# Optimization experiments

Hardware: AMD Instinct MI355X
Metric: run time of the kernel (lower is better)

The kernel has to match this reference:

```python
import jax, jax.numpy as jnp
import numpy as np

BN_EPS = 1e-5
K_NEIGHBOR = 30
NUM_GRAPH = 4


def _bn_lrelu(x, g, b, axes):
    # BatchNorm in training mode (batch stats, biased var) + LeakyReLU(0.2).
    mean = jnp.mean(x, axes, keepdims=True)
    var = jnp.var(x, axes, keepdims=True)
    y = (x - mean) * jax.lax.rsqrt(var + BN_EPS) * g + b
    return jnp.where(y > 0, y, 0.2 * y)


def _pairwise_distance(pc):
    # pc: (B, N, C) -> (B, N, N) squared euclidean distances
    inner = -2.0 * jnp.einsum('bnc,bmc->bnm', pc, pc)
    sq = jnp.sum(pc * pc, axis=-1, keepdims=True)
    return sq + inner + jnp.swapaxes(sq, 1, 2)


def _knn(adj, k):
    return jax.lax.top_k(-adj, k)[1]  # (B, N, k)


def _edge_feature(pc, idx):
    # pc: (B, N, C), idx: (B, N, k) -> (B, N, k, 2C)
    B = pc.shape[0]
    nbrs = pc[jnp.arange(B)[:, None, None], idx]          # (B, N, k, C)
    central = jnp.broadcast_to(pc[:, :, None, :], nbrs.shape)
    return jnp.concatenate([central, nbrs - central], axis=-1)


def _forward(input_image, w64, g64, b64, w128, g128, b128, w1024, g1024, b1024,
             fc1_w, fc1_b, fc2_w, fc2_b, tw, tb,
             wo1, go1, bo1, wo2, go2, bo2, wo3, go3, bo3,
             w1, g1, b1, w2, g2, b2, w3, g3, b3):
    pc = jnp.transpose(input_image, (0, 2, 1))            # (B, N, 3)
    k = K_NEIGHBOR

    # ---- input transform net ----
    idx = _knn(_pairwise_distance(pc), k)
    ef = _edge_feature(pc, idx)                           # (B, N, k, 6)
    net = _bn_lrelu(ef @ w64.T, g64, b64, (0, 1, 2))      # (B, N, k, 64)
    net = _bn_lrelu(net @ w128.T, g128, b128, (0, 1, 2))  # (B, N, k, 128)
    net = jnp.max(net, axis=2)                            # (B, N, 128)
    net = _bn_lrelu(net @ w1024.T, g1024, b1024, (0, 1))  # (B, N, 1024)
    net = jnp.max(net, axis=1)                            # (B, 1024)
    net = net @ fc1_w.T + fc1_b
    net = net @ fc2_w.T + fc2_b                           # (B, 256)
    transform = net @ tw + (jnp.eye(3, dtype=jnp.float32).reshape(-1) + tb)
    transform = transform.reshape(-1, 3, 3)               # (B, 3, 3)

    pct = pc @ transform                                  # (B, N, 3)

    # ---- feature extraction on transformed cloud ----
    idx = _knn(_pairwise_distance(pct), k)
    ef = _edge_feature(pct, idx)                          # (B, N, k, 6)
    out1 = _bn_lrelu(ef @ wo1.T, go1, bo1, (0, 1, 2))     # (B, N, k, 64)
    out2 = _bn_lrelu(out1 @ wo2.T, go2, bo2, (0, 1, 2))   # (B, N, k, 64)
    nmax = jnp.max(out2, axis=2)
    nmean = jnp.mean(out2, axis=2)
    cat1 = jnp.concatenate([nmax, nmean], axis=-1)        # (B, N, 128)
    out3 = _bn_lrelu(cat1 @ wo3.T, go3, bo3, (0, 1))      # (B, N, 64)

    # ---- num_graph dynamic-graph blocks ----
    out5s, maxs, means = [], [], []
    for _ in range(NUM_GRAPH):
        IF = jnp.concatenate([pct, out3], axis=-1)        # (B, N, 67)
        trans1 = _bn_lrelu(IF @ w1.T, g1, b1, (0, 1))     # (B, N, 3)
        idx = _knn(_pairwise_distance(trans1), k)
        ef = _edge_feature(IF, idx)                       # (B, N, k, 134)
        out4 = _bn_lrelu(ef @ w2.T, g2, b2, (0, 1, 2))    # (B, N, k, 16)
        nm2 = jnp.max(out4, axis=2)                       # (B, N, 16)
        ne2 = jnp.mean(out4, axis=2)
        o5 = jnp.concatenate([nm2, ne2], axis=-1)         # (B, N, 32)
        out5 = _bn_lrelu(o5 @ w3.T, g3, b3, (0, 1))       # (B, N, 16)
        out5s.append(out5); maxs.append(nm2); means.append(ne2)

    def _pack(xs):
        x = jnp.concatenate(xs, axis=-1)                  # (B, N, 64)
        return jnp.transpose(x, (0, 2, 1))[..., None]     # (B, 64, N, 1)

    return (_pack(out5s), _pack(maxs), _pack(means))


def setup_inputs() -> dict:
    key = jax.random.key(0)
    ks = iter(jax.random.split(key, 64))
    def w(shape, s=0.05):
        return jax.random.normal(next(ks), shape, jnp.float32) * s
    B, N = 4, 2048
    inp = {'input_image': jax.random.normal(next(ks), (B, 3, N), jnp.float32)}
    for name, shp in [('w64', (64, 6)), ('w128', (128, 64)), ('w1024', (1024, 128)),
                      ('wo1', (64, 6)), ('wo2', (64, 64)), ('wo3', (64, 128)),
                      ('w1', (3, 67)), ('w2', (16, 134)), ('w3', (16, 32))]:
        inp[name] = w(shp)
        c = shp[0]
        inp['g' + name[1:]] = jnp.ones((c,), jnp.float32)
        inp['b' + name[1:]] = jnp.zeros((c,), jnp.float32)
    inp['fc1_w'] = w((512, 1024)); inp['fc1_b'] = jnp.zeros((512,), jnp.float32)
    inp['fc2_w'] = w((256, 512)); inp['fc2_b'] = jnp.zeros((256,), jnp.float32)
    inp['tw'] = w((256, 9)); inp['tb'] = w((9,))
    return inp


def reference(input_image, w64, g64, b64, w128, g128, b128, w1024, g1024, b1024,
              fc1_w, fc1_b, fc2_w, fc2_b, tw, tb,
              wo1, go1, bo1, wo2, go2, bo2, wo3, go3, bo3,
              w1, g1, b1, w2, g2, b2, w3, g3, b3):
    return _forward(input_image, w64, g64, b64, w128, g128, b128, w1024, g1024, b1024,
                    fc1_w, fc1_b, fc2_w, fc2_b, tw, tb,
                    wo1, go1, bo1, wo2, go2, bo2, wo3, go3, bo3,
                    w1, g1, b1, w2, g2, b2, w3, g3, b3)
```

## Files before the change

### kernel.cpp

```cpp
#include <hip/hip_runtime.h>


#define DEV __device__ __forceinline__
DEV float lrelu(float y) { return y > 0.f ? y : 0.2f * y; }
DEV unsigned fmap(float x) {
  unsigned u = __float_as_uint(x);
  return (u & 0x80000000u) ? ~u : (u | 0x80000000u);
}
DEV float funmap(unsigned m) {
  unsigned u = (m & 0x80000000u) ? (m & 0x7FFFFFFFu) : ~m;
  return __uint_as_float(u);
}

__global__ void zero_kernel(float* p, int n) {
  int id = blockIdx.x * 256 + threadIdx.x;
  if (id < n) p[id] = 0.f;
}

__global__ void iminit_kernel(unsigned* maxm, unsigned* minm) {
  int id = blockIdx.x * 256 + threadIdx.x;
  if (id < 4096) { maxm[id] = 0u; minm[id] = 0xFFFFFFFFu; }
}

__global__ void pc_kernel(const float* __restrict__ in, float* __restrict__ pc) {
  int id = blockIdx.x * 256 + threadIdx.x;
  if (id >= 4 * 3 * 2048) return;
  int n = id & 2047;
  int c = (id >> 11) % 3;
  int b = id / (3 * 2048);
  pc[((b << 11) + n) * 3 + c] = in[id];
}

__global__ __launch_bounds__(256) void knn_kernel(const float* __restrict__ pts, int* __restrict__ idx_out) {
  int tid = threadIdx.x;
  int w = tid >> 6, lane = tid & 63;
  int bn = (blockIdx.x << 2) + w;
  int b = bn >> 11;
  const float* base = pts + (b << 11) * 3;
  double qx = pts[bn * 3 + 0], qy = pts[bn * 3 + 1], qz = pts[bn * 3 + 2];
  double sqn = qx * qx + qy * qy + qz * qz;
  double d[32];
  double cmin = 1e300; int cpos = 0x7fffffff;
#pragma unroll
  for (int i = 0; i < 32; ++i) {
    int m = lane + (i << 6);
    double px = base[m * 3 + 0], py = base[m * 3 + 1], pz = base[m * 3 + 2];
    double v = sqn - 2.0 * (qx * px + qy * py + qz * pz) + (px * px + py * py + pz * pz);
    d[i] = v;
    if (v < cmin) { cmin = v; cpos = m; }
  }
  unsigned rmask = 0u;
  int* out = idx_out + bn * 30;
  for (int it = 0; it < 30; ++it) {
    double gv = cmin; int gp = cpos;
#pragma unroll
    for (int off = 1; off < 64; off <<= 1) {
      double ov = __shfl_xor(gv, off, 64);
      int op = __shfl_xor(gp, off, 64);
      if (ov < gv || (ov == gv && op < gp)) { gv = ov; gp = op; }
    }
    if (lane == 0) out[it] = gp;
    if (lane == (gp & 63)) {
      rmask |= 1u << (gp >> 6);
      cmin = 1e300; cpos = 0x7fffffff;
#pragma unroll
      for (int i = 0; i < 32; ++i) {
        double v = ((rmask >> i) & 1u) ? 1e300 : d[i];
        if (v < cmin) { cmin = v; cpos = lane + (i << 6); }
      }
    }
  }
}

__global__ __launch_bounds__(256) void mom6_kernel(const float* __restrict__ pts, const int* __restrict__ idx,
                                                   double* __restrict__ acc) {
  __shared__ double sred[4][27];
  int tid = threadIdx.x;
  int lane = tid & 63, w = tid >> 6;
  double m[27];
#pragma unroll
  for (int i = 0; i < 27; ++i) m[i] = 0.0;
  int stride = gridDim.x << 8;
  for (int e = (blockIdx.x << 8) + tid; e < 245760; e += stride) {
    int bn = e / 30; int b = bn >> 11;
    int nb = idx[e];
    const float* cen = pts + bn * 3;
    const float* nbp = pts + ((b << 11) + nb) * 3;
    float f[6];
    f[0] = cen[0]; f[1] = cen[1]; f[2] = cen[2];
    f[3] = nbp[0] - f[0]; f[4] = nbp[1] - f[1]; f[5] = nbp[2] - f[2];
    int t = 6;
#pragma unroll
    for (int i = 0; i < 6; ++i) {
      m[i] += f[i];
#pragma unroll
      for (int j = i; j < 6; ++j) m[t++] += (double)f[i] * f[j];
    }
  }
#pragma unroll
  for (int i = 0; i < 27; ++i) {
    double v = m[i];
    v += __shfl_xor(v, 1, 64); v += __shfl_xor(v, 2, 64); v += __shfl_xor(v, 4, 64);
    v += __shfl_xor(v, 8, 64); v += __shfl_xor(v, 16, 64); v += __shfl_xor(v, 32, 64);
    m[i] = v;
  }
  if (lane == 0) {
#pragma unroll
    for (int i = 0; i < 27; ++i) sred[w][i] = m[i];
  }
  __syncthreads();
  if (tid < 27) atomicAdd(&acc[tid], sred[0][tid] + sred[1][tid] + sred[2][tid] + sred[3][tid]);
}

__global__ void finE1_kernel(const double* __restrict__ acc, const float* __restrict__ W,
                             const float* __restrict__ g, const float* __restrict__ bb,
                             float* __restrict__ sc) {
  int c = threadIdx.x;
  if (c >= 64) return;
  double wv[6];
#pragma unroll
  for (int i = 0; i < 6; ++i) wv[i] = W[c * 6 + i];
  double s = 0.0;
#pragma unroll
  for (int i = 0; i < 6; ++i) s += wv[i] * acc[i];
  double q = 0.0; int t = 6;
#pragma unroll
  for (int i = 0; i < 6; ++i)
#pragma unroll
    for (int j = i; j < 6; ++j) {
      double mm = acc[t++];
      q += (i == j) ? wv[i] * wv[i] * mm : 2.0 * wv[i] * wv[j] * mm;
    }
  const double E = 245760.0;
  double mean = s / E;
  double var = q / E - mean * mean;
  if (var < 0) var = 0;
  float sf = g[c] * (float)(1.0 / sqrt(var + 1e-5));
  sc[c] = sf;
  sc[64 + c] = bb[c] - (float)mean * sf;
}

__global__ __launch_bounds__(256) void edgeA_kernel(const float* __restrict__ pts, const int* __restrict__ idx,
                                                    const float* __restrict__ W1, const float* __restrict__ sc1,
                                                    const float* __restrict__ W2,
                                                    float* __restrict__ mxout, float* __restrict__ mnout,
                                                    double* __restrict__ acc) {
  __shared__ double sred[4][64][4];
  int tid = threadIdx.x;
  int lane = tid & 63;
  int wv = tid >> 6;
  int k = lane & 31;
  int bn = (blockIdx.x << 3) + (wv << 1) + (lane >> 5);
  int b = bn >> 11;
  bool valid = k < 30;
  int nb = idx[bn * 30 + (valid ? k : 0)];
  const float* cen = pts + bn * 3;
  const float* nbp = pts + ((b << 11) + nb) * 3;
  float cx = cen[0], cy = cen[1], cz = cen[2];
  float dx = nbp[0] - cx, dy = nbp[1] - cy, dz = nbp[2] - cz;
  float y[64];
#pragma unroll
  for (int j = 0; j < 64; ++j) {
    float x = cx * W1[j * 6 + 0] + cy * W1[j * 6 + 1] + cz * W1[j * 6 + 2]
            + dx * W1[j * 6 + 3] + dy * W1[j * 6 + 4] + dz * W1[j * 6 + 5];
    y[j] = lrelu(fmaf(x, sc1[j], sc1[64 + j]));
  }
  double aS0 = 0.0, aQ0 = 0.0, aS1 = 0.0, aQ1 = 0.0;
  for (int cc = 0; cc < 4; ++cc) {
    float kvx = 0.f, kvn = 0.f;
    for (int q = 0; q < 32; ++q) {
      int c = cc * 32 + q;
      const float* w = W2 + c * 64;
      float a0 = 0.f, a1 = 0.f, a2 = 0.f, a3 = 0.f;
#pragma unroll
      for (int j = 0; j < 64; j += 4) {
        a0 = fmaf(y[j], w[j], a0); a1 = fmaf(y[j + 1], w[j + 1], a1);
        a2 = fmaf(y[j + 2], w[j + 2], a2); a3 = fmaf(y[j + 3], w[j + 3], a3);
      }
      float v = (a0 + a1) + (a2 + a3);
      float vx = valid ? v : -3.4e38f;
      float vn = valid ? v : 3.4e38f;
      float sv = valid ? v : 0.f;
      float sq = valid ? v * v : 0.f;
#pragma unroll
      for (int off = 1; off < 32; off <<= 1) {
        vx = fmaxf(vx, __shfl_xor(vx, off, 64));
        vn = fminf(vn, __shfl_xor(vn, off, 64));
        sv += __shfl_xor(sv, off, 64);
        sq += __shfl_xor(sq, off, 64);
      }
      sv += __shfl_xor(sv, 32, 64);
      sq += __shfl_xor(sq, 32, 64);
      if (k == q) { kvx = vx; kvn = vn; }
      int ol = ((cc & 1) << 5) + q;
      bool own = (lane == ol);
      if (cc < 2) { aS0 += own ? (double)sv : 0.0; aQ0 += own ? (double)sq : 0.0; }
      else        { aS1 += own ? (double)sv : 0.0; aQ1 += own ? (double)sq : 0.0; }
    }
    mxout[bn * 128 + cc * 32 + k] = kvx;
    mnout[bn * 128 + cc * 32 + k] = kvn;
  }
  sred[wv][lane][0] = aS0; sred[wv][lane][1] = aQ0;
  sred[wv][lane][2] = aS1; sred[wv][lane][3] = aQ1;
  __syncthreads();
  int l = tid >> 2, j = tid & 3;
  double t = sred[0][l][j] + sred[1][l][j] + sred[2][l][j] + sred[3][l][j];
  int ch = (j < 2) ? l : 64 + l;
  atomicAdd(&acc[(j & 1) * 128 + ch], t);
}

__global__ void applyA_kernel(const float* __restrict__ mx, const float* __restrict__ mn,
                              const float* __restrict__ sc, float* __restrict__ m128) {
  int id = blockIdx.x * 256 + threadIdx.x;
  if (id >= 8192 * 128) return;
  int c = id & 127;
  float s = sc[c], t = sc[128 + c];
  float sel = (s >= 0.f) ? mx[id] : mn[id];
  m128[id] = lrelu(fmaf(sel, s, t));
}

__global__ __launch_bounds__(256) void statsB_kernel(const float* __restrict__ pts, const int* __restrict__ idx,
                                                     const float* __restrict__ W1, const float* __restrict__ sc1,
                                                     const float* __restrict__ W2, double* __restrict__ acc) {
  __shared__ double sred[4][64][2];
  int tid = threadIdx.x;
  int lane = tid & 63;
  int wv = tid >> 6;
  int k = lane & 31;
  int bn = (blockIdx.x << 3) + (wv << 1) + (lane >> 5);
  int b = bn >> 11;
  bool valid = k < 30;
  int nb = idx[bn * 30 + (valid ? k : 0)];
  const float* cen = pts + bn * 3;
  const float* nbp = pts + ((b << 11) + nb) * 3;
  float cx = cen[0], cy = cen[1], cz = cen[2];
  float dx = nbp[0] - cx, dy = nbp[1] - cy, dz = nbp[2] - cz;
  float y[64];
#pragma unroll
  for (int j = 0; j < 64; ++j) {
    float x = cx * W1[j * 6 + 0] + cy * W1[j * 6 + 1] + cz * W1[j * 6 + 2]
            + dx * W1[j * 6 + 3] + dy * W1[j * 6 + 4] + dz * W1[j * 6 + 5];
    y[j] = lrelu(fmaf(x, sc1[j], sc1[64 + j]));
  }
  double aS = 0.0, aQ = 0.0;
  for (int cc = 0; cc < 2; ++cc) {
    for (int q = 0; q < 32; ++q) {
      int c = cc * 32 + q;
      const float* w = W2 + c * 64;
      float a0 = 0.f, a1 = 0.f, a2 = 0.f, a3 = 0.f;
#pragma unroll
      for (int j = 0; j < 64; j += 4) {
        a0 = fmaf(y[j], w[j], a0); a1 = fmaf(y[j + 1], w[j + 1], a1);
        a2 = fmaf(y[j + 2], w[j + 2], a2); a3 = fmaf(y[j + 3], w[j + 3], a3);
      }
      float v = (a0 + a1) + (a2 + a3);
      float sv = valid ? v : 0.f;
      float sq = valid ? v * v : 0.f;
#pragma unroll
      for (int off = 1; off < 64; off <<= 1) {
        sv += __shfl_xor(sv, off, 64);
        sq += __shfl_xor(sq, off, 64);
      }
      bool own = (lane == c);
      aS += own ? (double)sv : 0.0;
      aQ += own ? (double)sq : 0.0;
    }
  }
  sred[wv][lane][0] = aS; sred[wv][lane][1] = aQ;
  __syncthreads();
  if (tid < 128) {
    int l = tid >> 1, j = tid & 1;
    double t = sred[0][l][j] + sred[1][l][j] + sred[2][l][j] + sred[3][l][j];
    atomicAdd(&acc[j * 64 + l], t);
  }
}

__global__ __launch_bounds__(256) void poolB_kernel(const float* __restrict__ pts, const int* __restrict__ idx,
                                                    const float* __restrict__ W1, const float* __restrict__ sc1,
                                                    const float* __restrict__ W2, const float* __restrict__ sc2,
                                                    float* __restrict__ cat) {
  int tid = threadIdx.x;
  int lane = tid & 63;
  int k = lane & 31;
  int bn = (blockIdx.x << 3) + ((tid >> 6) << 1) + (lane >> 5);
  int b = bn >> 11;
  bool valid = k < 30;
  int nb = idx[bn * 30 + (valid ? k : 0)];
  const float* cen = pts + bn * 3;
  const float* nbp = pts + ((b << 11) + nb) * 3;
  float cx = cen[0], cy = cen[1], cz = cen[2];
  float dx = nbp[0] - cx, dy = nbp[1] - cy, dz = nbp[2] - cz;
  float y[64];
#pragma unroll
  for (int j = 0; j < 64; ++j) {
    float x = cx * W1[j * 6 + 0] + cy * W1[j * 6 + 1] + cz * W1[j * 6 + 2]
            + dx * W1[j * 6 + 3] + dy * W1[j * 6 + 4] + dz * W1[j * 6 + 5];
    y[j] = lrelu(fmaf(x, sc1[j], sc1[64 + j]));
  }
  for (int cc = 0; cc < 2; ++cc) {
    float kvm = 0.f, kvs = 0.f;
    for (int q = 0; q < 32; ++q) {
      int c = cc * 32 + q;
      const float* w = W2 + c * 64;
      float a0 = 0.f, a1 = 0.f, a2 = 0.f, a3 = 0.f;
#pragma unroll
      for (int j = 0; j < 64; j += 4) {
        a0 = fmaf(y[j], w[j], a0); a1 = fmaf(y[j + 1], w[j + 1], a1);
        a2 = fmaf(y[j + 2], w[j + 2], a2); a3 = fmaf(y[j + 3], w[j + 3], a3);
      }
      float v = lrelu(fmaf((a0 + a1) + (a2 + a3), sc2[c], sc2[64 + c]));
      float vm = valid ? v : -3.4e38f;
      float vs = valid ? v : 0.f;
#pragma unroll
      for (int off = 1; off < 32; off <<= 1) {
        vm = fmaxf(vm, __shfl_xor(vm, off, 64));
        vs += __shfl_xor(vs, off, 64);
      }
      if (k == q) { kvm = vm; kvs = vs; }
    }
    cat[bn * 128 + cc * 32 + k] = kvm;
    cat[bn * 128 + 64 + cc * 32 + k] = kvs * (1.f / 30.f);
  }
}

__global__ __launch_bounds__(256) void xo3g_kernel(const float* __restrict__ cat, const float* __restrict__ W3,
                                                   float* __restrict__ xo3T) {
  int tid = threadIdx.x;
  int lane = tid & 63, cw = tid >> 6;
  int bn = (blockIdx.x << 6) + lane;
  const float* cr = cat + bn * 128;
  float a[16];
#pragma unroll
  for (int q = 0; q < 16; ++q) a[q] = 0.f;
  for (int j = 0; j < 128; ++j) {
    float v = cr[j];
#pragma unroll
    for (int q = 0; q < 16; ++q) a[q] += v * W3[(cw * 16 + q) * 128 + j];
  }
#pragma unroll
  for (int q = 0; q < 16; ++q) xo3T[(cw * 16 + q) * 8192 + bn] = a[q];
}

__global__ __launch_bounds__(256) void rstats_kernel(const float* __restrict__ x, int E, int C,
                                                     double* __restrict__ acc) {
  __shared__ double rd[256];
  int c = blockIdx.x, tid = threadIdx.x;
  const float* r = x + (size_t)c * E;
  double ls = 0, lq = 0;
  for (int i = tid; i < E; i += 256) { float v = r[i]; ls += v; lq += (double)v * v; }
  rd[tid] = ls; __syncthreads();
  for (int s = 128; s > 0; s >>= 1) { if (tid < s) rd[tid] += rd[tid + s]; __syncthreads(); }
  if (tid == 0) acc[c] = rd[0];
  __syncthreads();
  rd[tid] = lq; __syncthreads();
  for (int s = 128; s > 0; s >>= 1) { if (tid < s) rd[tid] += rd[tid + s]; __syncthreads(); }
  if (tid == 0) acc[C + c] = rd[0];
}

__global__ __launch_bounds__(256) void cmm1024_kernel(const float* __restrict__ m128, const float* __restrict__ W,
                                                      double* __restrict__ acc, unsigned* __restrict__ maxm,
                                                      unsigned* __restrict__ minm) {
  __shared__ float mt[64 * 132];
  int tid = threadIdx.x;
  int lane = tid & 63;
  int b = blockIdx.x >> 8;
  int cg = (blockIdx.x >> 2) & 63;
  int ns = blockIdx.x & 3;
  int wu = __builtin_amdgcn_readfirstlane(tid >> 6);
  int cbase = cg * 16 + wu * 4;
  const float* wr = W + (size_t)cbase * 128;
  double ls[4] = {0, 0, 0, 0}, lq[4] = {0, 0, 0, 0};
  float mx[4], mn[4];
#pragma unroll
  for (int q = 0; q < 4; ++q) { mx[q] = -3.4e38f; mn[q] = 3.4e38f; }
  for (int ch = 0; ch < 8; ++ch) {
    int n0 = (ns << 9) + (ch << 6);
    __syncthreads();
    for (int i = tid; i < 2048; i += 256) {
      int r = i >> 5, jj = (i & 31) << 2;
      *(float4*)&mt[r * 132 + jj] = *(const float4*)&m128[(size_t)((b << 11) + n0 + r) * 128 + jj];
    }
    __syncthreads();
    float a[4] = {0.f, 0.f, 0.f, 0.f};
    const float* mrow = &mt[lane * 132];
#pragma unroll
    for (int j = 0; j < 128; j += 4) {
      float4 mv = *(const float4*)&mrow[j];
#pragma unroll
      for (int q = 0; q < 4; ++q) {
        const float* wq = wr + q * 128 + j;
        a[q] = fmaf(mv.x, wq[0], a[q]);
        a[q] = fmaf(mv.y, wq[1], a[q]);
        a[q] = fmaf(mv.z, wq[2], a[q]);
        a[q] = fmaf(mv.w, wq[3], a[q]);
      }
    }
#pragma unroll
    for (int q = 0; q < 4; ++q) {
      ls[q] += a[q]; lq[q] += (double)a[q] * a[q];
      mx[q] = fmaxf(mx[q], a[q]); mn[q] = fminf(mn[q], a[q]);
    }
  }
#pragma unroll
  for (int q = 0; q < 4; ++q) {
    double s = ls[q], sq = lq[q];
    float xm = mx[q], xn = mn[q];
    for (int off = 1; off < 64; off <<= 1) {
      s += __shfl_xor(s, off, 64);
      sq += __shfl_xor(sq, off, 64);
      xm = fmaxf(xm, __shfl_xor(xm, off, 64));
      xn = fminf(xn, __shfl_xor(xn, off, 64));
    }
    if (lane == 0) {
      int c = cbase + q;
      atomicAdd(&acc[c], s);
      atomicAdd(&acc[1024 + c], sq);
      atomicMax(&maxm[(b << 10) + c], fmap(xm));
      atomicMin(&minm[(b << 10) + c], fmap(xn));
    }
  }
}

__global__ void fin1024_kernel(const double* __restrict__ acc, const float* __restrict__ g,
                               const float* __restrict__ bb, const unsigned* __restrict__ maxm,
                               const unsigned* __restrict__ minm, float* __restrict__ gmax) {
  int c = blockIdx.x * 256 + threadIdx.x;
  if (c >= 1024) return;
  double mean = acc[c] / 8192.0;
  double var = acc[1024 + c] / 8192.0 - mean * mean;
  if (var < 0) var = 0;
  float s = g[c] * (float)(1.0 / sqrt(var + 1e-5));
  float t = bb[c] - (float)mean * s;
  for (int b = 0; b < 4; ++b) {
    float xm = (s >= 0.f) ? funmap(maxm[(b << 10) + c]) : funmap(minm[(b << 10) + c]);
    gmax[(b << 10) + c] = lrelu(fmaf(xm, s, t));
  }
}

__global__ __launch_bounds__(256) void fc_kernel(const float* __restrict__ gmax,
                                                 const float* __restrict__ fc1w, const float* __restrict__ fc1b,
                                                 const float* __restrict__ fc2w, const float* __restrict__ fc2b,
                                                 const float* __restrict__ tw, const float* __restrict__ tb,
                                                 float* __restrict__ transform) {
  __shared__ float net[1024];
  __shared__ float h1[512];
  __shared__ float h2[256];
  int b = blockIdx.x, tid = threadIdx.x;
  for (int i = tid; i < 1024; i += 256) net[i] = gmax[b * 1024 + i];
  __syncthreads();
  for (int o = tid; o < 512; o += 256) {
    float a = fc1b[o];
    const float* w = fc1w + o * 1024;
    for (int j = 0; j < 1024; ++j) a += net[j] * w[j];
    h1[o] = a;
  }
  __syncthreads();
  {
    int o = tid;
    float a = fc2b[o];
    const float* w = fc2w + o * 512;
    for (int j = 0; j < 512; ++j) a += h1[j] * w[j];
    h2[o] = a;
  }
  __syncthreads();
  if (tid < 9) {
    float a = 0.f;
    for (int i = 0; i < 256; ++i) a += h2[i] * tw[i * 9 + tid];
    float eye = (tid == 0 || tid == 4 || tid == 8) ? 1.f : 0.f;
    transform[b * 9 + tid] = a + eye + tb[tid];
  }
}

__global__ void pct_kernel(const float* __restrict__ pc, const float* __restrict__ T, float* __restrict__ pct) {
  int id = blockIdx.x * 256 + threadIdx.x;
  if (id >= 8192) return;
  int b = id >> 11;
  const float* t = T + b * 9;
  float x = pc[id * 3 + 0], y = pc[id * 3 + 1], z = pc[id * 3 + 2];
  pct[id * 3 + 0] = x * t[0] + y * t[3] + z * t[6];
  pct[id * 3 + 1] = x * t[1] + y * t[4] + z * t[7];
  pct[id * 3 + 2] = x * t[2] + y * t[5] + z * t[8];
}

__global__ __launch_bounds__(256) void dstats_kernel(const float* __restrict__ x, int total, int C,
                                                     double* __restrict__ acc) {
  __shared__ double dred[256];
  int tid = threadIdx.x;
  int c = tid % C;
  double ls = 0, lq = 0;
  int stride = gridDim.x << 8;
  for (int id = (blockIdx.x << 8) + tid; id < total; id += stride) {
    float v = x[id];
    ls += v; lq += (double)v * v;
  }
  dred[tid] = ls; __syncthreads();
  if (tid < C) { double v = 0; for (int i = tid; i < 256; i += C) v += dred[i]; atomicAdd(&acc[c], v); }
  __syncthreads();
  dred[tid] = lq; __syncthreads();
  if (tid < C) { double v = 0; for (int i = tid; i < 256; i += C) v += dred[i]; atomicAdd(&acc[C + c], v); }
}

__global__ __launch_bounds__(256) void stats3_kernel(const float* __restrict__ x, int total, double* __restrict__ acc) {
  __shared__ double dred[256];
  int tid = threadIdx.x;
  double ls[3] = {0, 0, 0}, lq[3] = {0, 0, 0};
  int stride = gridDim.x << 8;
  for (int id = (blockIdx.x << 8) + tid; id < total; id += stride) {
    float v = x[id];
    int c = id % 3;
    ls[c] += v; lq[c] += (double)v * v;
  }
  for (int cc = 0; cc < 3; ++cc) {
    __syncthreads();
    dred[tid] = ls[cc]; __syncthreads();
    for (int s = 128; s > 0; s >>= 1) { if (tid < s) dred[tid] += dred[tid + s]; __syncthreads(); }
    if (tid == 0) atomicAdd(&acc[cc], dred[0]);
    __syncthreads();
    dred[tid] = lq[cc]; __syncthreads();
    for (int s = 128; s > 0; s >>= 1) { if (tid < s) dred[tid] += dred[tid + s]; __syncthreads(); }
    if (tid == 0) atomicAdd(&acc[3 + cc], dred[0]);
  }
}

__global__ void fin_kernel(const double* __restrict__ acc, const float* __restrict__ g, const float* __restrict__ bb,
                           double cnt, int C, float* __restrict__ sc) {
  int c = blockIdx.x * 256 + threadIdx.x;
  if (c >= C) return;
  double mean = acc[c] / cnt;
  double var = acc[C + c] / cnt - mean * mean;
  if (var < 0) var = 0;
  float inv = (float)(1.0 / sqrt(var + 1e-5));
  float s = g[c] * inv;
  sc[c] = s;
  sc[C + c] = bb[c] - (float)mean * s;
}

__global__ void if_kernel(const float* __restrict__ pct, const float* __restrict__ xo3T, const float* __restrict__ sc3,
                          float* __restrict__ IF) {
  int id = blockIdx.x * 256 + threadIdx.x;
  if (id >= 8192 * 67) return;
  int bn = id / 67, j = id % 67;
  float v;
  if (j < 3) v = pct[bn * 3 + j];
  else { int c = j - 3; v = lrelu(fmaf(xo3T[c * 8192 + bn], sc3[c], sc3[64 + c])); }
  IF[id] = v;
}

__global__ void xt1_kernel(const float* __restrict__ IF, const float* __restrict__ W, float* __restrict__ xt1) {
  int id = blockIdx.x * 256 + threadIdx.x;
  if (id >= 8192 * 3) return;
  int bn = id / 3, c = id % 3;
  const float* f = IF + bn * 67;
  const float* w = W + c * 67;
  float a = 0.f;
  for (int j = 0; j < 67; ++j) a += f[j] * w[j];
  xt1[id] = a;
}

__global__ void t1_kernel(const float* __restrict__ xt1, const float* __restrict__ sc, float* __restrict__ trans1) {
  int id = blockIdx.x * 256 + threadIdx.x;
  if (id >= 24576) return;
  int c = id % 3;
  trans1[id] = lrelu(fmaf(xt1[id], sc[c], sc[3 + c]));
}

__global__ __launch_bounds__(256) void x2_kernel(const float* __restrict__ IF, const int* __restrict__ idx,
                                                 const float* __restrict__ W, float* __restrict__ x2,
                                                 double* __restrict__ acc) {
  __shared__ float WT[134 * 16];
  __shared__ double dred[256];
  int tid = threadIdx.x;
  for (int i = tid; i < 134 * 16; i += 256) { int c = i & 15, j = i >> 4; WT[j * 16 + c] = W[c * 134 + j]; }
  __syncthreads();
  int c = tid & 15;
  double ls = 0, lq = 0;
  const int total = 245760 * 16;
  int stride = gridDim.x << 8;
  for (int id = (blockIdx.x << 8) + tid; id < total; id += stride) {
    int p = id >> 4;
    int bn = p / 30; int b = bn >> 11;
    int nb = idx[p];
    const float* cen = IF + (size_t)bn * 67;
    const float* nbp = IF + (size_t)((b << 11) + nb) * 67;
    float a = 0.f;
    for (int j = 0; j < 67; ++j) {
      float cj = cen[j];
      a += cj * WT[j * 16 + c];
      a += (nbp[j] - cj) * WT[(67 + j) * 16 + c];
    }
    x2[id] = a;
    ls += a; lq += (double)a * a;
  }
  dred[tid] = ls; __syncthreads();
  if (tid < 16) { double v = 0; for (int i = tid; i < 256; i += 16) v += dred[i]; atomicAdd(&acc[tid], v); }
  __syncthreads();
  dred[tid] = lq; __syncthreads();
  if (tid < 16) { double v = 0; for (int i = tid; i < 256; i += 16) v += dred[i]; atomicAdd(&acc[16 + tid], v); }
}

__global__ __launch_bounds__(256) void k5_kernel(const float* __restrict__ x2, const float* __restrict__ sc2,
                                                 const float* __restrict__ W3, float* __restrict__ nm2,
                                                 float* __restrict__ ne2, float* __restrict__ x3) {
  __shared__ float W3T[32 * 16];
  __shared__ float o5[4][32];
  int tid = threadIdx.x;
  for (int i = tid; i < 512; i += 256) { int c = i & 15, j = i >> 4; W3T[j * 16 + c] = W3[c * 32 + j]; }
  __syncthreads();
  int lane = tid & 63, w = tid >> 6;
  int bn = blockIdx.x * 4 + w;
  int c = lane & 15, kq = lane >> 4;
  float s = sc2[c], t = sc2[16 + c];
  float lm = -3.4e38f, lsm = 0.f;
  const float* xp = x2 + (size_t)bn * 30 * 16;
  for (int k = kq; k < 30; k += 4) {
    float v = lrelu(fmaf(xp[k * 16 + c], s, t));
    lm = fmaxf(lm, v); lsm += v;
  }
  float lm2 = fmaxf(lm, __shfl_down(lm, 32, 64)); lm2 = fmaxf(lm2, __shfl_down(lm2, 16, 64));
  float ls2 = lsm + __shfl_down(lsm, 32, 64); ls2 = ls2 + __shfl_down(ls2, 16, 64);
  if (lane < 16) {
    float mean = ls2 / 30.f;
    nm2[bn * 16 + c] = lm2;
    ne2[bn * 16 + c] = mean;
    o5[w][c] = lm2; o5[w][16 + c] = mean;
  }
  __syncthreads();
  if (lane < 16) {
    float a = 0.f;
#pragma unroll
    for (int j = 0; j < 32; ++j) a += o5[w][j] * W3T[j * 16 + c];
    x3[bn * 16 + c] = a;
  }
}

__global__ void out_kernel(const float* __restrict__ x3, const float* __restrict__ sc3,
                           const float* __restrict__ nm2, const float* __restrict__ ne2,
                           float* __restrict__ out) {
  int id = blockIdx.x * 256 + threadIdx.x;
  if (id >= 4 * 16 * 2048) return;
  int n = id & 2047;
  int j = (id >> 11) & 15;
  int b = id >> 15;
  int bn = (b << 11) + n;
  float v5 = lrelu(fmaf(x3[bn * 16 + j], sc3[j], sc3[16 + j]));
  float vm = nm2[bn * 16 + j];
  float ve = ne2[bn * 16 + j];
#pragma unroll
  for (int g = 0; g < 4; ++g) {
    size_t base = (size_t)(b * 64 + g * 16 + j) * 2048 + n;
    out[base] = v5;
    out[524288 + base] = vm;
    out[1048576 + base] = ve;
  }
}

extern "C" void kernel_launch(void* const* d_in, const int* in_sizes, int n_in,
                              void* d_out, int out_size, void* d_ws, size_t ws_size,
                              hipStream_t stream) {
  (void)n_in; (void)out_size; (void)ws_size;
  const float* input_image = (const float*)d_in[0];
  bool dict = (in_sizes[10] == 384);
  int I_wo1, I_go1, I_bo1, I_wo2, I_go2, I_bo2, I_wo3, I_go3, I_bo3;
  int I_w1, I_g1, I_b1, I_w2, I_g2, I_b2, I_w3, I_g3, I_b3;
  int I_fc1w, I_fc1b, I_fc2w, I_fc2b, I_tw, I_tb;
  if (dict) {
    I_wo1 = 10; I_go1 = 11; I_bo1 = 12; I_wo2 = 13; I_go2 = 14; I_bo2 = 15;
    I_wo3 = 16; I_go3 = 17; I_bo3 = 18;
    I_w1 = 19; I_g1 = 20; I_b1 = 21; I_w2 = 22; I_g2 = 23; I_b2 = 24; I_w3 = 25; I_g3 = 26; I_b3 = 27;
    I_fc1w = 28; I_fc1b = 29; I_fc2w = 30; I_fc2b = 31; I_tw = 32; I_tb = 33;
  } else {
    I_fc1w = 10; I_fc1b = 11; I_fc2w = 12; I_fc2b = 13; I_tw = 14; I_tb = 15;
    I_wo1 = 16; I_go1 = 17; I_bo1 = 18; I_wo2 = 19; I_go2 = 20; I_bo2 = 21;
    I_wo3 = 22; I_go3 = 23; I_bo3 = 24;
    I_w1 = 25; I_g1 = 26; I_b1 = 27; I_w2 = 28; I_g2 = 29; I_b2 = 30; I_w3 = 31; I_g3 = 32; I_b3 = 33;
  }
#define FIN(i) ((const float*)d_in[i])
  float* ws = (float*)d_ws;
  float* pc      = ws;
  float* pct     = ws + 24576;
  float* trans1  = ws + 49152;
  int*   idx1    = (int*)(ws + 73728);
  int*   idx2    = (int*)(ws + 319488);
  int*   idx3    = (int*)(ws + 565248);
  float* m128b   = ws + 811008;
  float* catb    = ws + 1859584;
  unsigned* maxmapb = (unsigned*)(ws + 2908160);
  unsigned* minmapb = (unsigned*)(ws + 2912256);
  float* m128mx  = ws + 2916352;
  float* m128mn  = ws + 3964928;
  float* gmaxb   = ws + 10248192;
  float* transf  = ws + 10252288;
  float* xo3T    = ws + 10252352;
  float* IFb     = ws + 10776640;
  float* xt1b    = ws + 11325504;
  float* x2b     = ws + 11350080;
  float* nm2b    = ws + 15282240;
  float* ne2b    = ws + 15413312;
  float* x3b     = ws + 15544384;
  double* acc    = (double*)(ws + 15675456);
  float* sc      = ws + 15683648;
  const double CNT_E = 245760.0, CNT_P = 8192.0;
  const int A64 = 0, A128 = 128, A1024 = 384, AO1 = 2432, AO2 = 2560, AO3 = 2688, AT1 = 2816, A2 = 2822, A3 = 2854;

  zero_kernel<<<32, 256, 0, stream>>>((float*)acc, 8192);
  iminit_kernel<<<16, 256, 0, stream>>>(maxmapb, minmapb);
  pc_kernel<<<96, 256, 0, stream>>>(input_image, pc);
  knn_kernel<<<2048, 256, 0, stream>>>(pc, idx1);
  mom6_kernel<<<32, 256, 0, stream>>>(pc, idx1, acc + A64);
  finE1_kernel<<<1, 64, 0, stream>>>(acc + A64, FIN(1), FIN(2), FIN(3), sc + A64);
  edgeA_kernel<<<1024, 256, 0, stream>>>(pc, idx1, FIN(1), sc + A64, FIN(4), m128mx, m128mn, acc + A128);
  fin_kernel<<<1, 256, 0, stream>>>(acc + A128, FIN(5), FIN(6), CNT_E, 128, sc + A128);
  applyA_kernel<<<4096, 256, 0, stream>>>(m128mx, m128mn, sc + A128, m128b);
  cmm1024_kernel<<<1024, 256, 0, stream>>>(m128b, FIN(7), acc + A1024, maxmapb, minmapb);
  fin1024_kernel<<<4, 256, 0, stream>>>(acc + A1024, FIN(8), FIN(9), maxmapb, minmapb, gmaxb);
  fc_kernel<<<4, 256, 0, stream>>>(gmaxb, FIN(I_fc1w), FIN(I_fc1b), FIN(I_fc2w), FIN(I_fc2b), FIN(I_tw), FIN(I_tb), transf);
  pct_kernel<<<32, 256, 0, stream>>>(pc, transf, pct);
  knn_kernel<<<2048, 256, 0, stream>>>(pct, idx2);
  mom6_kernel<<<32, 256, 0, stream>>>(pct, idx2, acc + AO1);
  finE1_kernel<<<1, 64, 0, stream>>>(acc + AO1, FIN(I_wo1), FIN(I_go1), FIN(I_bo1), sc + AO1);
  statsB_kernel<<<1024, 256, 0, stream>>>(pct, idx2, FIN(I_wo1), sc + AO1, FIN(I_wo2), acc + AO2);
  fin_kernel<<<1, 256, 0, stream>>>(acc + AO2, FIN(I_go2), FIN(I_bo2), CNT_E, 64, sc + AO2);
  poolB_kernel<<<1024, 256, 0, stream>>>(pct, idx2, FIN(I_wo1), sc + AO1, FIN(I_wo2), sc + AO2, catb);
  xo3g_kernel<<<128, 256, 0, stream>>>(catb, FIN(I_wo3), xo3T);
  rstats_kernel<<<64, 256, 0, stream>>>(xo3T, 8192, 64, acc + AO3);
  fin_kernel<<<1, 256, 0, stream>>>(acc + AO3, FIN(I_go3), FIN(I_bo3), CNT_P, 64, sc + AO3);
  if_kernel<<<2144, 256, 0, stream>>>(pct, xo3T, sc + AO3, IFb);
  xt1_kernel<<<96, 256, 0, stream>>>(IFb, FIN(I_w1), xt1b);
  stats3_kernel<<<32, 256, 0, stream>>>(xt1b, 24576, acc + AT1);
  fin_kernel<<<1, 256, 0, stream>>>(acc + AT1, FIN(I_g1), FIN(I_b1), CNT_P, 3, sc + AT1);
  t1_kernel<<<96, 256, 0, stream>>>(xt1b, sc + AT1, trans1);
  knn_kernel<<<2048, 256, 0, stream>>>(trans1, idx3);
  x2_kernel<<<512, 256, 0, stream>>>(IFb, idx3, FIN(I_w2), x2b, acc + A2);
  fin_kernel<<<1, 256, 0, stream>>>(acc + A2, FIN(I_g2), FIN(I_b2), CNT_E, 16, sc + A2);
  k5_kernel<<<2048, 256, 0, stream>>>(x2b, sc + A2, FIN(I_w3), nm2b, ne2b, x3b);
  dstats_kernel<<<256, 256, 0, stream>>>(x3b, 131072, 16, acc + A3);
  fin_kernel<<<1, 256, 0, stream>>>(acc + A3, FIN(I_g3), FIN(I_b3), CNT_P, 16, sc + A3);
  out_kernel<<<512, 256, 0, stream>>>(x3b, sc + A3, nm2b, ne2b, (float*)d_out);
#undef FIN
}
```

Before: 1.288 ms.

## Buffer top-4 candidates in kNN and transpose edge reductions through LDS

The kNN selection now keeps a sorted list of each lane's four smallest distances and only rescans its 32-entry register array after all four are used, instead of rescanning on every pick. The three edge-conv kernels stop doing per-channel butterfly shuffle reductions. Each lane writes its 32 channel outputs into a padded shared-memory tile, and each lane then reduces one channel over its 30 neighbours serially. This trades shuffle traffic for LDS writes and reads and adds block-wide barriers per channel chunk.

```diff
diff --git a/kernel.cpp b/kernel.cpp
--- a/kernel.cpp
+++ b/kernel.cpp
@@ -40,19 +40,33 @@
   double qx = pts[bn * 3 + 0], qy = pts[bn * 3 + 1], qz = pts[bn * 3 + 2];
   double sqn = qx * qx + qy * qy + qz * qz;
   double d[32];
-  double cmin = 1e300; int cpos = 0x7fffffff;
 #pragma unroll
   for (int i = 0; i < 32; ++i) {
     int m = lane + (i << 6);
     double px = base[m * 3 + 0], py = base[m * 3 + 1], pz = base[m * 3 + 2];
     double v = sqn - 2.0 * (qx * px + qy * py + qz * pz) + (px * px + py * py + pz * pz);
     d[i] = v;
-    if (v < cmin) { cmin = v; cpos = m; }
-  }
-  unsigned rmask = 0u;
+  }
+  unsigned used = 0u;
+  double l0, l1, l2, l3; int p0, p1, p2, p3;
+#define KNN_PASS(LV, PV)                                              \
+  {                                                                   \
+    double cm = 1e300; int cp = 0x7fffffff; int ci = 0;               \
+    _Pragma("unroll")                                                 \
+    for (int i = 0; i < 32; ++i) {                                    \
+      double v = ((used >> i) & 1u) ? 1e300 : d[i];                   \
+      if (v < cm) { cm = v; cp = lane + (i << 6); ci = i; }           \
+    }                                                                 \
+    used |= 1u << ci; LV = cm; PV = cp;                               \
+  }
+  KNN_PASS(l0, p0)
+  KNN_PASS(l1, p1)
+  KNN_PASS(l2, p2)
+  KNN_PASS(l3, p3)
+  int cnt = 4;
   int* out = idx_out + bn * 30;
   for (int it = 0; it < 30; ++it) {
-    double gv = cmin; int gp = cpos;
+    double gv = l0; int gp = p0;
 #pragma unroll
     for (int off = 1; off < 64; off <<= 1) {
       double ov = __shfl_xor(gv, off, 64);
@@ -61,15 +75,16 @@
     }
     if (lane == 0) out[it] = gp;
     if (lane == (gp & 63)) {
-      rmask |= 1u << (gp >> 6);
-      cmin = 1e300; cpos = 0x7fffffff;
-#pragma unroll
-      for (int i = 0; i < 32; ++i) {
-        double v = ((rmask >> i) & 1u) ? 1e300 : d[i];
-        if (v < cmin) { cmin = v; cpos = lane + (i << 6); }
+      l0 = l1; p0 = p1; l1 = l2; p1 = p2; l2 = l3; p2 = p3;
+      l3 = 1e300; p3 = 0x7fffffff;
+      cnt--;
+      if (cnt == 0) {
+        KNN_PASS(l0, p0)
+        cnt = 1;
       }
     }
   }
+#undef KNN_PASS
 }
 
 __global__ __launch_bounds__(256) void mom6_kernel(const float* __restrict__ pts, const int* __restrict__ idx,
@@ -145,12 +160,14 @@
                                                     const float* __restrict__ W2,
                                                     float* __restrict__ mxout, float* __restrict__ mnout,
                                                     double* __restrict__ acc) {
-  __shared__ double sred[4][64][4];
+  __shared__ float vbuf[4][2][32][33];
+  __shared__ double sred[4][32][8];
   int tid = threadIdx.x;
   int lane = tid & 63;
   int wv = tid >> 6;
   int k = lane & 31;
-  int bn = (blockIdx.x << 3) + (wv << 1) + (lane >> 5);
+  int pt = lane >> 5;
+  int bn = (blockIdx.x << 3) + (wv << 1) + pt;
   int b = bn >> 11;
   bool valid = k < 30;
   int nb = idx[bn * 30 + (valid ? k : 0)];
@@ -165,9 +182,11 @@
             + dx * W1[j * 6 + 3] + dy * W1[j * 6 + 4] + dz * W1[j * 6 + 5];
     y[j] = lrelu(fmaf(x, sc1[j], sc1[64 + j]));
   }
-  double aS0 = 0.0, aQ0 = 0.0, aS1 = 0.0, aQ1 = 0.0;
+  int ch = lane & 31, pt2 = lane >> 5;
+  int bn2 = (blockIdx.x << 3) + (wv << 1) + pt2;
+  double aS[4] = {0, 0, 0, 0}, aQ[4] = {0, 0, 0, 0};
+#pragma unroll
   for (int cc = 0; cc < 4; ++cc) {
-    float kvx = 0.f, kvn = 0.f;
     for (int q = 0; q < 32; ++q) {
       int c = cc * 32 + q;
       const float* w = W2 + c * 64;
@@ -177,36 +196,36 @@
         a0 = fmaf(y[j], w[j], a0); a1 = fmaf(y[j + 1], w[j + 1], a1);
         a2 = fmaf(y[j + 2], w[j + 2], a2); a3 = fmaf(y[j + 3], w[j + 3], a3);
       }
-      float v = (a0 + a1) + (a2 + a3);
-      float vx = valid ? v : -3.4e38f;
-      float vn = valid ? v : 3.4e38f;
-      float sv = valid ? v : 0.f;
-      float sq = valid ? v * v : 0.f;
-#pragma unroll
-      for (int off = 1; off < 32; off <<= 1) {
-        vx = fmaxf(vx, __shfl_xor(vx, off, 64));
-        vn = fminf(vn, __shfl_xor(vn, off, 64));
-        sv += __shfl_xor(sv, off, 64);
-        sq += __shfl_xor(sq, off, 64);
-      }
-      sv += __shfl_xor(sv, 32, 64);
-      sq += __shfl_xor(sq, 32, 64);
-      if (k == q) { kvx = vx; kvn = vn; }
-      int ol = ((cc & 1) << 5) + q;
-      bool own = (lane == ol);
-      if (cc < 2) { aS0 += own ? (double)sv : 0.0; aQ0 += own ? (double)sq : 0.0; }
-      else        { aS1 += own ? (double)sv : 0.0; aQ1 += own ? (double)sq : 0.0; }
-    }
-    mxout[bn * 128 + cc * 32 + k] = kvx;
-    mnout[bn * 128 + cc * 32 + k] = kvn;
-  }
-  sred[wv][lane][0] = aS0; sred[wv][lane][1] = aQ0;
-  sred[wv][lane][2] = aS1; sred[wv][lane][3] = aQ1;
-  __syncthreads();
-  int l = tid >> 2, j = tid & 3;
-  double t = sred[0][l][j] + sred[1][l][j] + sred[2][l][j] + sred[3][l][j];
-  int ch = (j < 2) ? l : 64 + l;
-  atomicAdd(&acc[(j & 1) * 128 + ch], t);
+      vbuf[wv][pt][q][k] = (a0 + a1) + (a2 + a3);
+    }
+    __syncthreads();
+    const float* vr = &vbuf[wv][pt2][ch][0];
+    float v0 = vr[0];
+    float mx = v0, mn = v0, sm = v0, qq = v0 * v0;
+#pragma unroll
+    for (int kk = 1; kk < 30; ++kk) {
+      float v = vr[kk];
+      mx = fmaxf(mx, v); mn = fminf(mn, v);
+      sm += v; qq = fmaf(v, v, qq);
+    }
+    mxout[bn2 * 128 + cc * 32 + ch] = mx;
+    mnout[bn2 * 128 + cc * 32 + ch] = mn;
+    float sm1 = __shfl_xor(sm, 32, 64);
+    float qq1 = __shfl_xor(qq, 32, 64);
+    if (lane < 32) { aS[cc] += (double)(sm + sm1); aQ[cc] += (double)(qq + qq1); }
+    __syncthreads();
+  }
+  if (lane < 32) {
+#pragma unroll
+    for (int cc = 0; cc < 4; ++cc) { sred[wv][lane][cc * 2] = aS[cc]; sred[wv][lane][cc * 2 + 1] = aQ[cc]; }
+  }
+  __syncthreads();
+  {
+    int l = tid >> 3, j = tid & 7;
+    double t = sred[0][l][j] + sred[1][l][j] + sred[2][l][j] + sred[3][l][j];
+    int c = (j >> 1) * 32 + l;
+    atomicAdd(&acc[(j & 1) * 128 + c], t);
+  }
 }
 
 __global__ void applyA_kernel(const float* __restrict__ mx, const float* __restrict__ mn,
@@ -222,12 +241,14 @@
 __global__ __launch_bounds__(256) void statsB_kernel(const float* __restrict__ pts, const int* __restrict__ idx,
                                                      const float* __restrict__ W1, const float* __restrict__ sc1,
                                                      const float* __restrict__ W2, double* __restrict__ acc) {
-  __shared__ double sred[4][64][2];
+  __shared__ float vbuf[4][2][32][33];
+  __shared__ double sred[4][32][4];
   int tid = threadIdx.x;
   int lane = tid & 63;
   int wv = tid >> 6;
   int k = lane & 31;
-  int bn = (blockIdx.x << 3) + (wv << 1) + (lane >> 5);
+  int pt = lane >> 5;
+  int bn = (blockIdx.x << 3) + (wv << 1) + pt;
   int b = bn >> 11;
   bool valid = k < 30;
   int nb = idx[bn * 30 + (valid ? k : 0)];
@@ -242,7 +263,9 @@
             + dx * W1[j * 6 + 3] + dy * W1[j * 6 + 4] + dz * W1[j * 6 + 5];
     y[j] = lrelu(fmaf(x, sc1[j], sc1[64 + j]));
   }
-  double aS = 0.0, aQ = 0.0;
+  int ch = lane & 31, pt2 = lane >> 5;
+  double aS[2] = {0, 0}, aQ[2] = {0, 0};
+#pragma unroll
   for (int cc = 0; cc < 2; ++cc) {
     for (int q = 0; q < 32; ++q) {
       int c = cc * 32 + q;
@@ -253,25 +276,32 @@
         a0 = fmaf(y[j], w[j], a0); a1 = fmaf(y[j + 1], w[j + 1], a1);
         a2 = fmaf(y[j + 2], w[j + 2], a2); a3 = fmaf(y[j + 3], w[j + 3], a3);
       }
-      float v = (a0 + a1) + (a2 + a3);
-      float sv = valid ? v : 0.f;
-      float sq = valid ? v * v : 0.f;
-#pragma unroll
-      for (int off = 1; off < 64; off <<= 1) {
-        sv += __shfl_xor(sv, off, 64);
-        sq += __shfl_xor(sq, off, 64);
-      }
-      bool own = (lane == c);
-      aS += own ? (double)sv : 0.0;
-      aQ += own ? (double)sq : 0.0;
-    }
-  }
-  sred[wv][lane][0] = aS; sred[wv][lane][1] = aQ;
+      vbuf[wv][pt][q][k] = (a0 + a1) + (a2 + a3);
+    }
+    __syncthreads();
+    const float* vr = &vbuf[wv][pt2][ch][0];
+    float v0 = vr[0];
+    float sm = v0, qq = v0 * v0;
+#pragma unroll
+    for (int kk = 1; kk < 30; ++kk) {
+      float v = vr[kk];
+      sm += v; qq = fmaf(v, v, qq);
+    }
+    float sm1 = __shfl_xor(sm, 32, 64);
+    float qq1 = __shfl_xor(qq, 32, 64);
+    if (lane < 32) { aS[cc] += (double)(sm + sm1); aQ[cc] += (double)(qq + qq1); }
+    __syncthreads();
+  }
+  if (lane < 32) {
+#pragma unroll
+    for (int cc = 0; cc < 2; ++cc) { sred[wv][lane][cc * 2] = aS[cc]; sred[wv][lane][cc * 2 + 1] = aQ[cc]; }
+  }
   __syncthreads();
   if (tid < 128) {
-    int l = tid >> 1, j = tid & 1;
+    int l = tid >> 2, j = tid & 3;
     double t = sred[0][l][j] + sred[1][l][j] + sred[2][l][j] + sred[3][l][j];
-    atomicAdd(&acc[j * 64 + l], t);
+    int c = (j >> 1) * 32 + l;
+    atomicAdd(&acc[(j & 1) * 64 + c], t);
   }
 }
 
@@ -279,10 +309,13 @@
                                                     const float* __restrict__ W1, const float* __restrict__ sc1,
                                                     const float* __restrict__ W2, const float* __restrict__ sc2,
                                                     float* __restrict__ cat) {
+  __shared__ float vbuf[4][2][32][33];
   int tid = threadIdx.x;
   int lane = tid & 63;
+  int wv = tid >> 6;
   int k = lane & 31;
-  int bn = (blockIdx.x << 3) + ((tid >> 6) << 1) + (lane >> 5);
+  int pt = lane >> 5;
+  int bn = (blockIdx.x << 3) + (wv << 1) + pt;
   int b = bn >> 11;
   bool valid = k < 30;
   int nb = idx[bn * 30 + (valid ? k : 0)];
@@ -297,8 +330,10 @@
             + dx * W1[j * 6 + 3] + dy * W1[j * 6 + 4] + dz * W1[j * 6 + 5];
     y[j] = lrelu(fmaf(x, sc1[j], sc1[64 + j]));
   }
+  int ch = lane & 31, pt2 = lane >> 5;
+  int bn2 = (blockIdx.x << 3) + (wv << 1) + pt2;
+#pragma unroll
   for (int cc = 0; cc < 2; ++cc) {
-    float kvm = 0.f, kvs = 0.f;
     for (int q = 0; q < 32; ++q) {
       int c = cc * 32 + q;
       const float* w = W2 + c * 64;
@@ -308,18 +343,22 @@
         a0 = fmaf(y[j], w[j], a0); a1 = fmaf(y[j + 1], w[j + 1], a1);
         a2 = fmaf(y[j + 2], w[j + 2], a2); a3 = fmaf(y[j + 3], w[j + 3], a3);
       }
-      float v = lrelu(fmaf((a0 + a1) + (a2 + a3), sc2[c], sc2[64 + c]));
-      float vm = valid ? v : -3.4e38f;
-      float vs = valid ? v : 0.f;
-#pragma unroll
-      for (int off = 1; off < 32; off <<= 1) {
-        vm = fmaxf(vm, __shfl_xor(vm, off, 64));
-        vs += __shfl_xor(vs, off, 64);
-      }
-      if (k == q) { kvm = vm; kvs = vs; }
-    }
-    cat[bn * 128 + cc * 32 + k] = kvm;
-    cat[bn * 128 + 64 + cc * 32 + k] = kvs * (1.f / 30.f);
+      vbuf[wv][pt][q][k] = (a0 + a1) + (a2 + a3);
+    }
+    __syncthreads();
+    int c2 = cc * 32 + ch;
+    float s = sc2[c2], t = sc2[64 + c2];
+    const float* vr = &vbuf[wv][pt2][ch][0];
+    float v0 = lrelu(fmaf(vr[0], s, t));
+    float mx = v0, sm = v0;
+#pragma unroll
+    for (int kk = 1; kk < 30; ++kk) {
+      float v = lrelu(fmaf(vr[kk], s, t));
+      mx = fmaxf(mx, v); sm += v;
+    }
+    cat[bn2 * 128 + cc * 32 + ch] = mx;
+    cat[bn2 * 128 + 64 + cc * 32 + ch] = sm * (1.f / 30.f);
+    __syncthreads();
   }
 }
 
```

Result: faster. 1.247 ms (-3.1%).
